# Kernel tuning notes

Measured on AMD Instinct MI355X. Metric: run time of the kernel, lower is better.

The kernel has to match this reference:

```python
import jax, jax.numpy as jnp
import numpy as np

B, S, NT, D, NU = 1024, 200, 10000, 256, 100000
BETA_1 = 0.1


def setup_inputs() -> dict:
    key = jax.random.key(0)
    ks = jax.random.split(key, 6)
    user_id = jax.random.randint(ks[0], (B,), 0, NU)
    event_type = jax.random.randint(ks[1], (B, S), 0, NT + 1)  # 0 = pad
    adjacent_matrix = jax.random.uniform(ks[2], (NT, NT), dtype=jnp.float32)
    pop_encoding = jax.random.normal(ks[3], (NT + 1, D), dtype=jnp.float32)
    event_emb = jax.random.normal(ks[4], (NT + 1, D), dtype=jnp.float32) * 0.02
    user_emb = jax.random.normal(ks[5], (NU, D), dtype=jnp.float32) * 0.02
    return dict(user_id=user_id, event_type=event_type,
                adjacent_matrix=adjacent_matrix, pop_encoding=pop_encoding,
                evaluation=0, event_emb=event_emb, user_emb=user_emb)


def _l2norm(x, eps):
    # tf.nn.l2_normalize: x * rsqrt(max(sum(x^2), eps))
    return x * jax.lax.rsqrt(jnp.maximum(jnp.sum(x * x, axis=-1, keepdims=True), eps))


def reference(user_id, event_type, adjacent_matrix, pop_encoding, evaluation, event_emb, user_emb):
    non_pad = (event_type != 0).astype(jnp.float32)[..., None]          # [B,S,1]
    enc = event_emb[event_type]                                          # [B,S,D]
    usr = user_emb[user_id]                                              # [B,D]
    pop = pop_encoding[event_type] * non_pad                             # [B,S,D]
    # enc += sign(enc) * l2_normalize(user_output) (default eps 1e-12)
    enc = enc + jnp.sign(enc) * _l2norm(usr, 1e-12)[:, None, :]
    # per-sample adjacency: two-axis gather of the item-item matrix
    idx = jnp.where(event_type > 0, event_type - 1, 0)                   # [B,S]
    adj = adjacent_matrix[idx[:, :, None], idx[:, None, :]]              # [B,S,S]
    has_valid = (jnp.sum(event_type > 0, axis=1) > 0).astype(jnp.float32)
    adj = adj * has_valid[:, None, None]  # rows with all-pad stay zero, as in the loop
    output = jnp.mean(enc, axis=1)                                       # [B,D]
    user_embeddings = jnp.concatenate([output, jnp.mean(pop, axis=1) * BETA_1], axis=-1)  # [B,2D]
    if evaluation:
        item_encoding = event_emb[1:]                                    # [NT,D]
        scores = user_embeddings[:, :D] @ item_encoding.T
    else:
        item_encoding = jnp.concatenate([event_emb[1:], pop_encoding[1:] * BETA_1], axis=-1)  # [NT,2D]
        scores = user_embeddings @ item_encoding.T                       # [B,NT]
    prediction = jnp.tanh(_l2norm(scores, 1e-05))
    return prediction, user_embeddings, pop, adj
```

## Files before the change

kernel.cpp:

```cpp
#include <hip/hip_runtime.h>
#include <math.h>

#define NB 1024
#define NS 200
#define NTOK 10000
#define ND 256
#define BETA 0.1f

static constexpr size_t PRED_OFF = 0;
static constexpr size_t UE_OFF   = (size_t)NB * NTOK;
static constexpr size_t POP_OFF  = UE_OFF + (size_t)NB * 2 * ND;
static constexpr size_t ADJ_OFF  = POP_OFF + (size_t)NB * NS * ND;

static constexpr size_t WS_SIDX   = 0;
static constexpr size_t WS_HV     = WS_SIDX + (size_t)NB * NS;
static constexpr size_t WS_COUNTS = WS_HV + NB;
static constexpr size_t WS_OFFS   = WS_COUNTS + NTOK;
static constexpr size_t WS_CURSOR = WS_OFFS + NTOK + 1;
static constexpr size_t WS_PAIRS  = WS_CURSOR + NTOK;
static constexpr size_t WS_UEBF   = 440640;
static constexpr size_t WS_IEBF   = WS_UEBF + 262144;

typedef __attribute__((ext_vector_type(8))) short bf16x8;
typedef __attribute__((ext_vector_type(4))) float f32x4;
typedef __attribute__((ext_vector_type(8))) unsigned short u16x8;

static __device__ inline unsigned short f2bf(float f) {
    unsigned int u = __float_as_uint(f);
    return (unsigned short)((u + 0x7fffu + ((u >> 16) & 1u)) >> 16);
}

__global__ __launch_bounds__(256) void k_front(
    const int* __restrict__ user_id,
    const int* __restrict__ event_type,
    const float* __restrict__ pop_encoding,
    const float* __restrict__ event_emb,
    const float* __restrict__ user_emb,
    float* __restrict__ ue,
    unsigned short* __restrict__ ue_bf,
    float* __restrict__ pop,
    int* __restrict__ sidx_all,
    float* __restrict__ hvf,
    unsigned short* __restrict__ ie)
{
    const int t = threadIdx.x;

    if (blockIdx.x >= NB) {
        const int idx = (blockIdx.x - NB) * 256 + t;
        const int row = idx >> 7;
        const int kq  = idx & 127;
        float4 v; float sc;
        if (kq < 64) { v = *(const float4*)&event_emb[(size_t)(row + 1) * ND + kq * 4]; sc = 1.f; }
        else         { v = *(const float4*)&pop_encoding[(size_t)(row + 1) * ND + (kq - 64) * 4]; sc = BETA; }
        ushort4 h = {f2bf(v.x * sc), f2bf(v.y * sc), f2bf(v.z * sc), f2bf(v.w * sc)};
        *(ushort4*)&ie[(size_t)row * 512 + kq * 4] = h;
        return;
    }

    const int b  = blockIdx.x;
    const int sg = t >> 6;
    const int tl = t & 63;

    const int uid = user_id[b];
    const float4 u4 = *(const float4*)&user_emb[(size_t)uid * ND + tl * 4];

    float ss = u4.x * u4.x + u4.y * u4.y + u4.z * u4.z + u4.w * u4.w;
    #pragma unroll
    for (int o = 32; o > 0; o >>= 1) ss += __shfl_xor(ss, o, 64);
    const float rn = rsqrtf(fmaxf(ss, 1e-12f));
    const float4 nu4 = {u4.x * rn, u4.y * rn, u4.z * rn, u4.w * rn};

    __shared__ int et_s[NS];
    __shared__ int hv_s;
    if (t == 0) hv_s = 0;
    if (t < NS) et_s[t] = event_type[(size_t)b * NS + t];
    __syncthreads();

    if (t < NS) {
        const int et = et_s[t];
        sidx_all[(size_t)b * NS + t] = (et > 0) ? (et - 1) : 0;
        if (et > 0) hv_s = 1;
    }

    float4 eacc = {0.f, 0.f, 0.f, 0.f};
    float4 pacc = {0.f, 0.f, 0.f, 0.f};
    #pragma unroll 2
    for (int it = 0; it < NS / 4; ++it) {
        const int s  = sg + 4 * it;
        const int et = et_s[s];
        const float4 e = *(const float4*)&event_emb[(size_t)et * ND + tl * 4];
        float4 p = *(const float4*)&pop_encoding[(size_t)et * ND + tl * 4];
        const float z = (et != 0) ? 1.f : 0.f;
        p.x *= z; p.y *= z; p.z *= z; p.w *= z;
        eacc.x += e.x + ((e.x > 0.f) ? nu4.x : ((e.x < 0.f) ? -nu4.x : 0.f));
        eacc.y += e.y + ((e.y > 0.f) ? nu4.y : ((e.y < 0.f) ? -nu4.y : 0.f));
        eacc.z += e.z + ((e.z > 0.f) ? nu4.z : ((e.z < 0.f) ? -nu4.z : 0.f));
        eacc.w += e.w + ((e.w > 0.f) ? nu4.w : ((e.w < 0.f) ? -nu4.w : 0.f));
        pacc.x += p.x; pacc.y += p.y; pacc.z += p.z; pacc.w += p.w;
        const f32x4 pv = {p.x, p.y, p.z, p.w};
        __builtin_nontemporal_store(pv, (f32x4*)&pop[((size_t)b * NS + s) * ND + tl * 4]);
    }

    __shared__ __align__(16) float4 es[4][64];
    __shared__ __align__(16) float4 ps[4][64];
    es[sg][tl] = eacc;
    ps[sg][tl] = pacc;
    __syncthreads();

    if (t < 128) {
        const int half = t >> 6;
        const int l2   = t & 63;
        float4 f = half ? ps[0][l2] : es[0][l2];
        #pragma unroll
        for (int w = 1; w < 4; ++w) {
            const float4 g = half ? ps[w][l2] : es[w][l2];
            f.x += g.x; f.y += g.y; f.z += g.z; f.w += g.w;
        }
        const float sc = half ? (BETA / NS) : (1.f / NS);
        const float4 o = {f.x * sc, f.y * sc, f.z * sc, f.w * sc};
        const size_t off = (size_t)b * 512 + half * 256 + l2 * 4;
        *(float4*)&ue[off] = o;
        ushort4 h = {f2bf(o.x), f2bf(o.y), f2bf(o.z), f2bf(o.w)};
        *(ushort4*)&ue_bf[off] = h;
    }
    if (t == 0) hvf[b] = hv_s ? 1.f : 0.f;
}

#define SCAN_CHUNK 40
__global__ __launch_bounds__(256) void k_scan(
    const int* __restrict__ sidx_all,
    int* __restrict__ offsets,
    int* __restrict__ cursor)
{
    const int t = threadIdx.x;
    __shared__ int cnt[NTOK];
    for (int i = t; i < NTOK; i += 256) cnt[i] = 0;
    __syncthreads();

    const int4* s4 = (const int4*)sidx_all;
    for (int i = t; i < NB * NS / 4; i += 256) {
        const int4 v = s4[i];
        atomicAdd(&cnt[v.x], 1);
        atomicAdd(&cnt[v.y], 1);
        atomicAdd(&cnt[v.z], 1);
        atomicAdd(&cnt[v.w], 1);
    }
    __syncthreads();

    int sum = 0;
    int local[SCAN_CHUNK];
    #pragma unroll
    for (int k = 0; k < SCAN_CHUNK; ++k) {
        const int idx = t * SCAN_CHUNK + k;
        const int c = (idx < NTOK) ? cnt[idx] : 0;
        local[k] = c;
        sum += c;
    }
    __shared__ int part[256];
    part[t] = sum;
    __syncthreads();
    for (int o = 1; o < 256; o <<= 1) {
        const int v = (t >= o) ? part[t - o] : 0;
        __syncthreads();
        part[t] += v;
        __syncthreads();
    }
    int running = part[t] - sum;
    #pragma unroll
    for (int k = 0; k < SCAN_CHUNK; ++k) {
        const int idx = t * SCAN_CHUNK + k;
        if (idx < NTOK) {
            offsets[idx] = running;
            cursor[idx]  = running;
            running += local[k];
        }
    }
    if (t == 255) offsets[NTOK] = part[255];
}

__global__ __launch_bounds__(256) void k_scatter(
    const int* __restrict__ sidx_all,
    int* __restrict__ cursor,
    int* __restrict__ pairs)
{
    const int b = blockIdx.x;
    const int t = threadIdx.x;
    if (t < NS) {
        const int r = sidx_all[(size_t)b * NS + t];
        const int slot = atomicAdd(&cursor[r], 1);
        pairs[slot] = b * NS + t;
    }
}

#define GBM 128
#define GBN 128
#define GBK 32
#define LDK 40
#define NGEMM 632

__global__ __launch_bounds__(256) void k_main(
    const unsigned short* __restrict__ ue_bf,
    const unsigned short* __restrict__ ie_bf,
    float* __restrict__ scores,
    const float* __restrict__ A,
    const int* __restrict__ sidx_all,
    const int* __restrict__ offsets,
    const int* __restrict__ pairs,
    const float* __restrict__ hvf,
    float* __restrict__ adj)
{
    __shared__ __align__(16) unsigned char smem[40960];
    const int t = threadIdx.x;

    if (blockIdx.x < NGEMM) {
        unsigned short* As = (unsigned short*)smem;
        unsigned short* Bs = As + GBM * LDK;

        const int g  = blockIdx.x;
        const int bn = g % 79, bm = g / 79;
        const int m0 = bm * GBM, n0 = bn * GBN;

        const int wave = t >> 6, lane = t & 63;
        const int ww = wave & 1, wm = wave >> 1;
        const int lr = lane & 15;
        const int kg = lane >> 4;

        f32x4 acc[4][4] = {};

        for (int k0 = 0; k0 < 512; k0 += GBK) {
            #pragma unroll
            for (int i = 0; i < 2; ++i) {
                const int c = t + 256 * i;
                const int row = c >> 2, q = c & 3;
                *(u16x8*)&As[row * LDK + q * 8] =
                    *(const u16x8*)&ue_bf[(size_t)(m0 + row) * 512 + k0 + q * 8];
            }
            #pragma unroll
            for (int i = 0; i < 2; ++i) {
                const int c = t + 256 * i;
                const int row = c >> 2, q = c & 3;
                const int gn = n0 + row;
                u16x8 h = {0, 0, 0, 0, 0, 0, 0, 0};
                if (gn < NTOK)
                    h = *(const u16x8*)&ie_bf[(size_t)gn * 512 + k0 + q * 8];
                *(u16x8*)&Bs[row * LDK + q * 8] = h;
            }
            __syncthreads();

            bf16x8 a[4], b[4];
            #pragma unroll
            for (int mf = 0; mf < 4; ++mf)
                a[mf] = *(const bf16x8*)&As[(wm * 64 + mf * 16 + lr) * LDK + kg * 8];
            #pragma unroll
            for (int nf = 0; nf < 4; ++nf)
                b[nf] = *(const bf16x8*)&Bs[(ww * 64 + nf * 16 + lr) * LDK + kg * 8];
            #pragma unroll
            for (int mf = 0; mf < 4; ++mf)
                #pragma unroll
                for (int nf = 0; nf < 4; ++nf)
                    acc[mf][nf] = __builtin_amdgcn_mfma_f32_16x16x32_bf16(
                        a[mf], b[nf], acc[mf][nf], 0, 0, 0);
            __syncthreads();
        }

        #pragma unroll
        for (int mf = 0; mf < 4; ++mf) {
            const int row = m0 + wm * 64 + mf * 16 + kg * 4;
            #pragma unroll
            for (int nf = 0; nf < 4; ++nf) {
                const int col = n0 + ww * 64 + nf * 16 + lr;
                if (col < NTOK) {
                    #pragma unroll
                    for (int r = 0; r < 4; ++r)
                        scores[(size_t)(row + r) * NTOK + col] = acc[mf][nf][r];
                }
            }
        }
        return;
    }

    const int r = blockIdx.x - NGEMM;
    const int p0 = offsets[r];
    const int n  = offsets[r + 1] - p0;
    if (n == 0) return;

    float* rowlds = (float*)smem;
    const float4* Arow = (const float4*)(A + (size_t)r * NTOK);
    #pragma unroll 4
    for (int l = t; l < NTOK / 4; l += 256)
        ((float4*)rowlds)[l] = Arow[l];
    __syncthreads();

    const int wave = t >> 6, lane = t & 63;
    for (int pi = wave; pi < n; pi += 4) {
        const int pv = pairs[p0 + pi];
        const int b  = pv / NS;
        const float hv = hvf[b];
        if (lane < 50) {
            const int4 c4 = *(const int4*)&sidx_all[(size_t)b * NS + lane * 4];
            f32x4 v;
            v.x = rowlds[c4.x] * hv;
            v.y = rowlds[c4.y] * hv;
            v.z = rowlds[c4.z] * hv;
            v.w = rowlds[c4.w] * hv;
            __builtin_nontemporal_store(v, (f32x4*)&adj[(size_t)pv * NS + lane * 4]);
        }
    }
}

__global__ __launch_bounds__(256) void k_norm(float* __restrict__ scores)
{
    const int b = blockIdx.x;
    const int t = threadIdx.x;
    float4* row4 = (float4*)(scores + (size_t)b * NTOK);

    float ss = 0.f;
    for (int l = t; l < NTOK / 4; l += 256) {
        const float4 v = row4[l];
        ss += v.x * v.x + v.y * v.y + v.z * v.z + v.w * v.w;
    }
    #pragma unroll
    for (int o = 32; o > 0; o >>= 1) ss += __shfl_down(ss, o, 64);
    __shared__ float wss[4];
    const int wid = t >> 6, lane = t & 63;
    if (lane == 0) wss[wid] = ss;
    __syncthreads();
    const float tot = wss[0] + wss[1] + wss[2] + wss[3];
    const float rs = rsqrtf(fmaxf(tot, 1e-5f));

    for (int l = t; l < NTOK / 4; l += 256) {
        float4 v = row4[l];
        v.x = tanhf(v.x * rs); v.y = tanhf(v.y * rs);
        v.z = tanhf(v.z * rs); v.w = tanhf(v.w * rs);
        row4[l] = v;
    }
}

extern "C" void kernel_launch(void* const* d_in, const int* in_sizes, int n_in,
                              void* d_out, int out_size, void* d_ws, size_t ws_size,
                              hipStream_t stream) {
    const int*   user_id      = (const int*)d_in[0];
    const int*   event_type   = (const int*)d_in[1];
    const float* adjacent     = (const float*)d_in[2];
    const float* pop_encoding = (const float*)d_in[3];
    const float* event_emb    = (const float*)d_in[5];
    const float* user_emb     = (const float*)d_in[6];

    float* out  = (float*)d_out;
    float* pred = out + PRED_OFF;
    float* ue   = out + UE_OFF;
    float* pop  = out + POP_OFF;
    float* adj  = out + ADJ_OFF;

    int*   ws       = (int*)d_ws;
    int*   sidx_all = ws + WS_SIDX;
    float* hvf      = (float*)(ws + WS_HV);
    int*   offsets  = ws + WS_OFFS;
    int*   cursor   = ws + WS_CURSOR;
    int*   pairs    = ws + WS_PAIRS;
    unsigned short* ue_bf = (unsigned short*)(ws + WS_UEBF);
    unsigned short* ie_bf = (unsigned short*)(ws + WS_IEBF);

    k_front<<<NB + 5000, 256, 0, stream>>>(user_id, event_type, pop_encoding,
                                           event_emb, user_emb, ue, ue_bf, pop,
                                           sidx_all, hvf, ie_bf);
    k_scan<<<1, 256, 0, stream>>>(sidx_all, offsets, cursor);
    k_scatter<<<NB, 256, 0, stream>>>(sidx_all, cursor, pairs);
    k_main<<<NGEMM + NTOK, 256, 0, stream>>>(ue_bf, ie_bf, pred,
                                             adjacent, sidx_all, offsets, pairs,
                                             hvf, adj);
    k_norm<<<NB, 256, 0, stream>>>(pred);
}
```

Measured before the change: 370.6 us.

## Split fused GEMM/adjacency kernel into separate launches with flattened adjacency work

The combined kernel that ran GEMM blocks and adjacency-gather blocks side by side is split into two launches: a 512-thread adjacency kernel and a standalone MFMA GEMM kernel on a 2D grid. In the adjacency kernel each thread handles one (pair, 4-column chunk) unit, so no lanes sit idle, and the row is loaded with nontemporal loads. Shared memory is sized per kernel instead of using a union, which may change occupancy. In exchange the two workloads no longer overlap within a single launch, and an extra kernel launch is added.

Result: faster. 350.8 us (-5.4%).

```diff
diff --git a/kernel.cpp b/kernel.cpp
--- a/kernel.cpp
+++ b/kernel.cpp
@@ -192,16 +192,7 @@
     }
 }
 
-#define GBM 128
-#define GBN 128
-#define GBK 32
-#define LDK 40
-#define NGEMM 632
-
-__global__ __launch_bounds__(256) void k_main(
-    const unsigned short* __restrict__ ue_bf,
-    const unsigned short* __restrict__ ie_bf,
-    float* __restrict__ scores,
+__global__ __launch_bounds__(512) void k_adj2(
     const float* __restrict__ A,
     const int* __restrict__ sidx_all,
     const int* __restrict__ offsets,
@@ -209,101 +200,109 @@
     const float* __restrict__ hvf,
     float* __restrict__ adj)
 {
-    __shared__ __align__(16) unsigned char smem[40960];
-    const int t = threadIdx.x;
-
-    if (blockIdx.x < NGEMM) {
-        unsigned short* As = (unsigned short*)smem;
-        unsigned short* Bs = As + GBM * LDK;
-
-        const int g  = blockIdx.x;
-        const int bn = g % 79, bm = g / 79;
-        const int m0 = bm * GBM, n0 = bn * GBN;
-
-        const int wave = t >> 6, lane = t & 63;
-        const int ww = wave & 1, wm = wave >> 1;
-        const int lr = lane & 15;
-        const int kg = lane >> 4;
-
-        f32x4 acc[4][4] = {};
-
-        for (int k0 = 0; k0 < 512; k0 += GBK) {
-            #pragma unroll
-            for (int i = 0; i < 2; ++i) {
-                const int c = t + 256 * i;
-                const int row = c >> 2, q = c & 3;
-                *(u16x8*)&As[row * LDK + q * 8] =
-                    *(const u16x8*)&ue_bf[(size_t)(m0 + row) * 512 + k0 + q * 8];
-            }
-            #pragma unroll
-            for (int i = 0; i < 2; ++i) {
-                const int c = t + 256 * i;
-                const int row = c >> 2, q = c & 3;
-                const int gn = n0 + row;
-                u16x8 h = {0, 0, 0, 0, 0, 0, 0, 0};
-                if (gn < NTOK)
-                    h = *(const u16x8*)&ie_bf[(size_t)gn * 512 + k0 + q * 8];
-                *(u16x8*)&Bs[row * LDK + q * 8] = h;
-            }
-            __syncthreads();
-
-            bf16x8 a[4], b[4];
-            #pragma unroll
-            for (int mf = 0; mf < 4; ++mf)
-                a[mf] = *(const bf16x8*)&As[(wm * 64 + mf * 16 + lr) * LDK + kg * 8];
-            #pragma unroll
-            for (int nf = 0; nf < 4; ++nf)
-                b[nf] = *(const bf16x8*)&Bs[(ww * 64 + nf * 16 + lr) * LDK + kg * 8];
-            #pragma unroll
-            for (int mf = 0; mf < 4; ++mf)
-                #pragma unroll
-                for (int nf = 0; nf < 4; ++nf)
-                    acc[mf][nf] = __builtin_amdgcn_mfma_f32_16x16x32_bf16(
-                        a[mf], b[nf], acc[mf][nf], 0, 0, 0);
-            __syncthreads();
-        }
-
-        #pragma unroll
-        for (int mf = 0; mf < 4; ++mf) {
-            const int row = m0 + wm * 64 + mf * 16 + kg * 4;
-            #pragma unroll
-            for (int nf = 0; nf < 4; ++nf) {
-                const int col = n0 + ww * 64 + nf * 16 + lr;
-                if (col < NTOK) {
-                    #pragma unroll
-                    for (int r = 0; r < 4; ++r)
-                        scores[(size_t)(row + r) * NTOK + col] = acc[mf][nf][r];
-                }
-            }
-        }
-        return;
-    }
-
-    const int r = blockIdx.x - NGEMM;
+    const int r = blockIdx.x;
+    const int t = threadIdx.x;
     const int p0 = offsets[r];
     const int n  = offsets[r + 1] - p0;
     if (n == 0) return;
 
-    float* rowlds = (float*)smem;
-    const float4* Arow = (const float4*)(A + (size_t)r * NTOK);
-    #pragma unroll 4
-    for (int l = t; l < NTOK / 4; l += 256)
-        ((float4*)rowlds)[l] = Arow[l];
-    __syncthreads();
-
-    const int wave = t >> 6, lane = t & 63;
-    for (int pi = wave; pi < n; pi += 4) {
+    __shared__ __align__(16) float rowlds[NTOK];
+    const f32x4* Arow = (const f32x4*)(A + (size_t)r * NTOK);
+    #pragma unroll 5
+    for (int l = t; l < NTOK / 4; l += 512) {
+        const f32x4 v = __builtin_nontemporal_load(&Arow[l]);
+        *(f32x4*)&rowlds[l * 4] = v;
+    }
+    __syncthreads();
+
+    const int nunits = n * 50;
+    for (int l = t; l < nunits; l += 512) {
+        const int pi = l / 50;
+        const int q  = l - pi * 50;
         const int pv = pairs[p0 + pi];
         const int b  = pv / NS;
         const float hv = hvf[b];
-        if (lane < 50) {
-            const int4 c4 = *(const int4*)&sidx_all[(size_t)b * NS + lane * 4];
-            f32x4 v;
-            v.x = rowlds[c4.x] * hv;
-            v.y = rowlds[c4.y] * hv;
-            v.z = rowlds[c4.z] * hv;
-            v.w = rowlds[c4.w] * hv;
-            __builtin_nontemporal_store(v, (f32x4*)&adj[(size_t)pv * NS + lane * 4]);
+        const int4 c4 = *(const int4*)&sidx_all[(size_t)b * NS + q * 4];
+        f32x4 v;
+        v.x = rowlds[c4.x] * hv;
+        v.y = rowlds[c4.y] * hv;
+        v.z = rowlds[c4.z] * hv;
+        v.w = rowlds[c4.w] * hv;
+        __builtin_nontemporal_store(v, (f32x4*)&adj[(size_t)pv * NS + q * 4]);
+    }
+}
+
+#define GBM 128
+#define GBN 128
+#define GBK 32
+#define LDK 40
+
+__global__ __launch_bounds__(256) void k_gemm_mfma(
+    const unsigned short* __restrict__ ue_bf,
+    const unsigned short* __restrict__ ie_bf,
+    float* __restrict__ scores)
+{
+    __shared__ __align__(16) unsigned short As[GBM * LDK];
+    __shared__ __align__(16) unsigned short Bs[GBN * LDK];
+
+    const int t  = threadIdx.x;
+    const int bn = blockIdx.x, bm = blockIdx.y;
+    const int m0 = bm * GBM, n0 = bn * GBN;
+
+    const int wave = t >> 6, lane = t & 63;
+    const int ww = wave & 1, wm = wave >> 1;
+    const int lr = lane & 15;
+    const int kg = lane >> 4;
+
+    f32x4 acc[4][4] = {};
+
+    for (int k0 = 0; k0 < 512; k0 += GBK) {
+        #pragma unroll
+        for (int i = 0; i < 2; ++i) {
+            const int c = t + 256 * i;
+            const int row = c >> 2, q = c & 3;
+            *(u16x8*)&As[row * LDK + q * 8] =
+                *(const u16x8*)&ue_bf[(size_t)(m0 + row) * 512 + k0 + q * 8];
+        }
+        #pragma unroll
+        for (int i = 0; i < 2; ++i) {
+            const int c = t + 256 * i;
+            const int row = c >> 2, q = c & 3;
+            const int gn = n0 + row;
+            u16x8 h = {0, 0, 0, 0, 0, 0, 0, 0};
+            if (gn < NTOK)
+                h = *(const u16x8*)&ie_bf[(size_t)gn * 512 + k0 + q * 8];
+            *(u16x8*)&Bs[row * LDK + q * 8] = h;
+        }
+        __syncthreads();
+
+        bf16x8 a[4], b[4];
+        #pragma unroll
+        for (int mf = 0; mf < 4; ++mf)
+            a[mf] = *(const bf16x8*)&As[(wm * 64 + mf * 16 + lr) * LDK + kg * 8];
+        #pragma unroll
+        for (int nf = 0; nf < 4; ++nf)
+            b[nf] = *(const bf16x8*)&Bs[(ww * 64 + nf * 16 + lr) * LDK + kg * 8];
+        #pragma unroll
+        for (int mf = 0; mf < 4; ++mf)
+            #pragma unroll
+            for (int nf = 0; nf < 4; ++nf)
+                acc[mf][nf] = __builtin_amdgcn_mfma_f32_16x16x32_bf16(
+                    a[mf], b[nf], acc[mf][nf], 0, 0, 0);
+        __syncthreads();
+    }
+
+    #pragma unroll
+    for (int mf = 0; mf < 4; ++mf) {
+        const int row = m0 + wm * 64 + mf * 16 + kg * 4;
+        #pragma unroll
+        for (int nf = 0; nf < 4; ++nf) {
+            const int col = n0 + ww * 64 + nf * 16 + lr;
+            if (col < NTOK) {
+                #pragma unroll
+                for (int r = 0; r < 4; ++r)
+                    scores[(size_t)(row + r) * NTOK + col] = acc[mf][nf][r];
+            }
         }
     }
 }
@@ -366,8 +365,8 @@
                                            sidx_all, hvf, ie_bf);
     k_scan<<<1, 256, 0, stream>>>(sidx_all, offsets, cursor);
     k_scatter<<<NB, 256, 0, stream>>>(sidx_all, cursor, pairs);
-    k_main<<<NGEMM + NTOK, 256, 0, stream>>>(ue_bf, ie_bf, pred,
-                                             adjacent, sidx_all, offsets, pairs,
-                                             hvf, adj);
+    k_adj2<<<NTOK, 512, 0, stream>>>(adjacent, sidx_all, offsets, pairs, hvf, adj);
+    dim3 ggrid((NTOK + GBN - 1) / GBN, NB / GBM);
+    k_gemm_mfma<<<ggrid, 256, 0, stream>>>(ue_bf, ie_bf, pred);
     k_norm<<<NB, 256, 0, stream>>>(pred);
 }
```
